# Kernel tuning notes

Measured on AMD Instinct MI355X. Metric: run time of the kernel, lower is better.

The kernel has to match this reference:

```python
import jax, jax.numpy as jnp
import numpy as np

N_NODES = 50000
N_EDGES = 800000
IN_F = 128
HEADS = 8
HEAD_DIM = 16
ALPHA = 0.2  # LeakyReLU negative slope
EPS = 1e-6


def setup_inputs() -> dict:
    key = jax.random.key(0)
    k1, k2, k3, k4 = jax.random.split(key, 4)
    x = jax.random.normal(k1, (N_NODES, IN_F), dtype=jnp.float32)
    edge_index = jax.random.randint(k2, (2, N_EDGES), 0, N_NODES, dtype=jnp.int32)
    std = 1.0 / np.sqrt(IN_F)
    W = jax.random.uniform(k3, (HEADS, IN_F, HEAD_DIM), minval=-std, maxval=std, dtype=jnp.float32)
    a = jax.random.uniform(k4, (HEADS, 2 * HEAD_DIM, 1), minval=-std, maxval=std, dtype=jnp.float32)
    bias = jnp.zeros((HEADS * HEAD_DIM,), dtype=jnp.float32)
    return {"x": x, "edge_index": edge_index, "W": W, "a": a, "bias": bias}


def reference(x, edge_index, W, a, bias):
    N = x.shape[0]
    src = edge_index[0]
    tgt = edge_index[1]
    # per-head linear transform: [N, H, D]
    h = jnp.einsum('nf,hfd->nhd', x, W)
    # split attention vector: a = [a_src; a_tgt], each [H, D]
    a_src = a[:, :HEAD_DIM, 0]
    a_tgt = a[:, HEAD_DIM:, 0]
    # node-level partial scores, then gather (equivalent to concat@a on edges)
    s_node_src = jnp.einsum('nhd,hd->nh', h, a_src)  # [N, H]
    s_node_tgt = jnp.einsum('nhd,hd->nh', h, a_tgt)  # [N, H]
    scores = s_node_src[src] + s_node_tgt[tgt]       # [E, H]
    scores = jnp.where(scores >= 0, scores, ALPHA * scores)  # LeakyReLU
    # edge softmax per target node, per head (global max subtract + clamp, as in source)
    max_per_head = jnp.max(scores, axis=0, keepdims=True)    # [1, H]
    exp_scores = jnp.exp(jnp.clip(scores - max_per_head, -20.0, 20.0))  # [E, H]
    denom = jax.ops.segment_sum(exp_scores, tgt, num_segments=N) + EPS  # [N, H]
    attn = exp_scores / denom[tgt]                                      # [E, H]
    # weighted scatter-add aggregation
    weighted = h[src] * attn[:, :, None]                                # [E, H, D]
    agg = jax.ops.segment_sum(weighted, tgt, num_segments=N)            # [N, H, D]
    out = agg.reshape(N, HEADS * HEAD_DIM) + bias
    return out
```

## Files before the change

### kernel.cpp

```cpp
#include <hip/hip_runtime.h>
#include <stdint.h>

#define N_NODES 50000
#define N_EDGES 800000
#define IN_F 128
#define HEADS 8
#define HEAD_DIM 16
#define ALPHA 0.2f
#define EPSV 1e-6f

#define NB 196
#define CAP 4800

typedef short short8 __attribute__((ext_vector_type(8)));
typedef float floatx4 __attribute__((ext_vector_type(4)));

__device__ __forceinline__ float bflo(unsigned v) {
    return __uint_as_float(v << 16);
}
__device__ __forceinline__ float bfhi(unsigned v) {
    return __uint_as_float(v & 0xffff0000u);
}
__device__ __forceinline__ unsigned f2bf(float f) {
    unsigned u = __float_as_uint(f);
    return (u + 0x7fffu + ((u >> 16) & 1u)) >> 16;
}

__global__ __launch_bounds__(256) void k_wt(const float* __restrict__ W,
                                            ushort* __restrict__ WTb,
                                            int* __restrict__ gcnt) {
    int i = blockIdx.x * 256 + threadIdx.x;
    int c = i >> 7, f = i & 127;
    WTb[i] = (ushort)f2bf(W[(c >> 4) * 2048 + f * 16 + (c & 15)]);
    if (i < NB) gcnt[i] = 0;
}

__global__ __launch_bounds__(256) void k_mid(const float* __restrict__ x,
                                             const ushort* __restrict__ WTb,
                                             const float* __restrict__ a,
                                             ushort* __restrict__ hb,
                                             float* __restrict__ s_src,
                                             float* __restrict__ s_tgt,
                                             const int* __restrict__ srcA,
                                             const int* __restrict__ tgtA,
                                             int* __restrict__ gcnt,
                                             unsigned* __restrict__ bucketbuf) {
    int bi = blockIdx.x;
    int q3 = bi / 3, r3 = bi - q3 * 3;
    int t = threadIdx.x;

    if (r3 == 2) {
        __shared__ int lcnt[NB];
        __shared__ int lbase[NB];
        if (t < NB) lcnt[t] = 0;
        __syncthreads();

        int base = q3 * 2048 + t;
        int tg[8], sr[8];
        bool vld[8];
#pragma unroll
        for (int k = 0; k < 8; k++) {
            int e = base + k * 256;
            vld[k] = (e < N_EDGES);
            int ee = vld[k] ? e : 0;
            tg[k] = tgtA[ee];
            sr[k] = srcA[ee];
        }
#pragma unroll
        for (int k = 0; k < 8; k++)
            if (vld[k]) atomicAdd(&lcnt[tg[k] >> 8], 1);
        __syncthreads();
        if (t < NB) {
            int c = lcnt[t];
            lbase[t] = (c > 0) ? atomicAdd(&gcnt[t], c) : 0;
            lcnt[t] = 0;
        }
        __syncthreads();
#pragma unroll
        for (int k = 0; k < 8; k++) {
            if (vld[k]) {
                int b = tg[k] >> 8;
                int off = atomicAdd(&lcnt[b], 1);
                int pos = lbase[b] + off;
                if (pos < CAP)
                    bucketbuf[(size_t)b * CAP + pos] =
                        ((unsigned)(tg[k] & 255) << 16) | (unsigned)sr[k];
            }
        }
        return;
    }

    int mb = q3 * 2 + r3;
    int wave = t >> 6, lane = t & 63;
    int quad = lane >> 4, col = lane & 15;
    int nb = mb * 64 + wave * 16;

    int na = nb + col;
    int nac = na < N_NODES ? na : (N_NODES - 1);
    const float* xrow = x + (size_t)nac * 128 + quad * 8;

    floatx4 acc[8];
    floatx4 z = {0.f, 0.f, 0.f, 0.f};
#pragma unroll
    for (int ct = 0; ct < 8; ct++) acc[ct] = z;

#pragma unroll
    for (int kc = 0; kc < 4; kc++) {
        float4 f0 = *(const float4*)(xrow + kc * 32);
        float4 f1 = *(const float4*)(xrow + kc * 32 + 4);
        short8 af;
        af[0] = (short)f2bf(f0.x); af[1] = (short)f2bf(f0.y);
        af[2] = (short)f2bf(f0.z); af[3] = (short)f2bf(f0.w);
        af[4] = (short)f2bf(f1.x); af[5] = (short)f2bf(f1.y);
        af[6] = (short)f2bf(f1.z); af[7] = (short)f2bf(f1.w);
#pragma unroll
        for (int ct = 0; ct < 8; ct++) {
            const ushort* wrow = WTb + (size_t)(ct * 16 + col) * 128 + kc * 32 + quad * 8;
            short8 bf = *(const short8*)wrow;
            acc[ct] = __builtin_amdgcn_mfma_f32_16x16x32_bf16(af, bf, acc[ct], 0, 0, 0);
        }
    }

    float af_s[8], af_t[8];
#pragma unroll
    for (int ct = 0; ct < 8; ct++) {
        af_s[ct] = a[ct * 32 + col];
        af_t[ct] = a[ct * 32 + 16 + col];
    }

#pragma unroll
    for (int r = 0; r < 4; r++) {
        int node = nb + quad * 4 + r;
        bool nv = (node < N_NODES);
        if (nv) {
            ushort* hrow = hb + (size_t)node * 128 + col;
#pragma unroll
            for (int ct = 0; ct < 8; ct++)
                hrow[ct * 16] = (ushort)f2bf(acc[ct][r]);
        }
        float ps[8], pt[8];
#pragma unroll
        for (int ct = 0; ct < 8; ct++) {
            float hs = acc[ct][r];
            float vs = hs * af_s[ct];
            float vt = hs * af_t[ct];
#pragma unroll
            for (int off = 1; off < 16; off <<= 1) {
                vs += __shfl_xor(vs, off, 64);
                vt += __shfl_xor(vt, off, 64);
            }
            ps[ct] = vs; pt[ct] = vt;
        }
        if (nv && col == 0) {
            *(float4*)(s_src + (size_t)node * 8)     = make_float4(ps[0], ps[1], ps[2], ps[3]);
            *(float4*)(s_src + (size_t)node * 8 + 4) = make_float4(ps[4], ps[5], ps[6], ps[7]);
            *(float4*)(s_tgt + (size_t)node * 8)     = make_float4(pt[0], pt[1], pt[2], pt[3]);
            *(float4*)(s_tgt + (size_t)node * 8 + 4) = make_float4(pt[4], pt[5], pt[6], pt[7]);
        }
    }
}

__global__ __launch_bounds__(256) void k_passB(const unsigned* __restrict__ bucketbuf,
                                               const int* __restrict__ gcnt,
                                               int* __restrict__ rowptr,
                                               ushort* __restrict__ src16) {
    __shared__ int bin[256];
    __shared__ int wsum[4];
    __shared__ int woff[4];
    __shared__ int sbase;
    __shared__ ushort stage[CAP];
    int t = threadIdx.x, lane = t & 63, w = t >> 6;
    int b = blockIdx.x;

    bin[t] = 0;
    int g = (t < NB) ? gcnt[t] : 0;
    int incg = g;
#pragma unroll
    for (int off = 1; off < 64; off <<= 1) {
        int nn = __shfl_up(incg, off, 64);
        if (lane >= off) incg += nn;
    }
    if (lane == 63) wsum[w] = incg;
    __syncthreads();
    if (t == 0) {
        woff[0] = 0;
        woff[1] = wsum[0];
        woff[2] = wsum[0] + wsum[1];
        woff[3] = wsum[0] + wsum[1] + wsum[2];
    }
    __syncthreads();
    if (t == b) sbase = woff[w] + incg - g;
    if (b == 0 && t == 0) rowptr[N_NODES] = N_EDGES;
    __syncthreads();
    int base = sbase;
    int n = gcnt[b]; if (n > CAP) n = CAP;
    const unsigned* buf = bucketbuf + (size_t)b * CAP;

    for (int i = t; i < n; i += 256)
        atomicAdd(&bin[buf[i] >> 16], 1);
    __syncthreads();
    int v = bin[t];
    int inc = v;
#pragma unroll
    for (int off = 1; off < 64; off <<= 1) {
        int nn = __shfl_up(inc, off, 64);
        if (lane >= off) inc += nn;
    }
    if (lane == 63) wsum[w] = inc;
    __syncthreads();
    if (t == 0) {
        woff[0] = 0;
        woff[1] = wsum[0];
        woff[2] = wsum[0] + wsum[1];
        woff[3] = wsum[0] + wsum[1] + wsum[2];
    }
    __syncthreads();
    int excl = woff[w] + inc - v;
    int node = b * 256 + t;
    if (node < N_NODES) rowptr[node] = base + excl;
    __syncthreads();
    bin[t] = excl;
    __syncthreads();
    for (int i = t; i < n; i += 256) {
        unsigned p = buf[i];
        int off = atomicAdd(&bin[p >> 16], 1);
        stage[off] = (ushort)(p & 0xffffu);
    }
    __syncthreads();
    for (int i = t; i < n; i += 256)
        src16[base + i] = stage[i];
}

__global__ __launch_bounds__(256) void k_fused(const int* __restrict__ rowptr,
                                               const ushort* __restrict__ src16,
                                               const float* __restrict__ s_src,
                                               const float* __restrict__ s_tgt,
                                               const unsigned* __restrict__ h16,
                                               const float* __restrict__ bias,
                                               float* __restrict__ outb) {
    int t = threadIdx.x;
    int wave = t >> 6, lane = t & 63;
    int half = lane >> 5, hl = lane & 31;
    int n = blockIdx.x * 8 + wave * 2 + half;
    int head = hl >> 2;
    int c = 4 * hl;

    const uint2* h2 = (const uint2*)h16;

    float st = s_tgt[n * 8 + head];
    int begin = rowptr[n], end = rowptr[n + 1];

    float ax = 0.f, ay = 0.f, az = 0.f, aw = 0.f, den = 0.f;
    int e = begin;
    for (; e + 7 < end; e += 8) {
        int s0 = src16[e];
        int s1 = src16[e + 1];
        int s2 = src16[e + 2];
        int s3 = src16[e + 3];
        int s4 = src16[e + 4];
        int s5 = src16[e + 5];
        int s6 = src16[e + 6];
        int s7 = src16[e + 7];
        float t0 = s_src[s0 * 8 + head];
        float t1 = s_src[s1 * 8 + head];
        float t2 = s_src[s2 * 8 + head];
        float t3 = s_src[s3 * 8 + head];
        float t4 = s_src[s4 * 8 + head];
        float t5 = s_src[s5 * 8 + head];
        float t6 = s_src[s6 * 8 + head];
        float t7 = s_src[s7 * 8 + head];
        uint2 p0 = h2[s0 * 32 + hl];
        uint2 p1 = h2[s1 * 32 + hl];
        uint2 p2 = h2[s2 * 32 + hl];
        uint2 p3 = h2[s3 * 32 + hl];
        uint2 p4 = h2[s4 * 32 + hl];
        uint2 p5 = h2[s5 * 32 + hl];
        uint2 p6 = h2[s6 * 32 + hl];
        uint2 p7 = h2[s7 * 32 + hl];
        float v0 = t0 + st; v0 = v0 >= 0.f ? v0 : ALPHA * v0;
        float v1 = t1 + st; v1 = v1 >= 0.f ? v1 : ALPHA * v1;
        float v2 = t2 + st; v2 = v2 >= 0.f ? v2 : ALPHA * v2;
        float v3 = t3 + st; v3 = v3 >= 0.f ? v3 : ALPHA * v3;
        float v4 = t4 + st; v4 = v4 >= 0.f ? v4 : ALPHA * v4;
        float v5 = t5 + st; v5 = v5 >= 0.f ? v5 : ALPHA * v5;
        float v6 = t6 + st; v6 = v6 >= 0.f ? v6 : ALPHA * v6;
        float v7 = t7 + st; v7 = v7 >= 0.f ? v7 : ALPHA * v7;
        float x0 = __expf(fminf(fmaxf(v0, -20.f), 20.f));
        float x1 = __expf(fminf(fmaxf(v1, -20.f), 20.f));
        float x2 = __expf(fminf(fmaxf(v2, -20.f), 20.f));
        float x3 = __expf(fminf(fmaxf(v3, -20.f), 20.f));
        float x4 = __expf(fminf(fmaxf(v4, -20.f), 20.f));
        float x5 = __expf(fminf(fmaxf(v5, -20.f), 20.f));
        float x6 = __expf(fminf(fmaxf(v6, -20.f), 20.f));
        float x7 = __expf(fminf(fmaxf(v7, -20.f), 20.f));
        den += ((x0 + x1) + (x2 + x3)) + ((x4 + x5) + (x6 + x7));
        ax = fmaf(x0, bflo(p0.x), fmaf(x1, bflo(p1.x), fmaf(x2, bflo(p2.x), fmaf(x3, bflo(p3.x), ax))));
        ax = fmaf(x4, bflo(p4.x), fmaf(x5, bflo(p5.x), fmaf(x6, bflo(p6.x), fmaf(x7, bflo(p7.x), ax))));
        ay = fmaf(x0, bfhi(p0.x), fmaf(x1, bfhi(p1.x), fmaf(x2, bfhi(p2.x), fmaf(x3, bfhi(p3.x), ay))));
        ay = fmaf(x4, bfhi(p4.x), fmaf(x5, bfhi(p5.x), fmaf(x6, bfhi(p6.x), fmaf(x7, bfhi(p7.x), ay))));
        az = fmaf(x0, bflo(p0.y), fmaf(x1, bflo(p1.y), fmaf(x2, bflo(p2.y), fmaf(x3, bflo(p3.y), az))));
        az = fmaf(x4, bflo(p4.y), fmaf(x5, bflo(p5.y), fmaf(x6, bflo(p6.y), fmaf(x7, bflo(p7.y), az))));
        aw = fmaf(x0, bfhi(p0.y), fmaf(x1, bfhi(p1.y), fmaf(x2, bfhi(p2.y), fmaf(x3, bfhi(p3.y), aw))));
        aw = fmaf(x4, bfhi(p4.y), fmaf(x5, bfhi(p5.y), fmaf(x6, bfhi(p6.y), fmaf(x7, bfhi(p7.y), aw))));
    }
    if (e + 3 < end) {
        int s0 = src16[e];
        int s1 = src16[e + 1];
        int s2 = src16[e + 2];
        int s3 = src16[e + 3];
        float t0 = s_src[s0 * 8 + head];
        float t1 = s_src[s1 * 8 + head];
        float t2 = s_src[s2 * 8 + head];
        float t3 = s_src[s3 * 8 + head];
        uint2 p0 = h2[s0 * 32 + hl];
        uint2 p1 = h2[s1 * 32 + hl];
        uint2 p2 = h2[s2 * 32 + hl];
        uint2 p3 = h2[s3 * 32 + hl];
        float v0 = t0 + st; v0 = v0 >= 0.f ? v0 : ALPHA * v0;
        float v1 = t1 + st; v1 = v1 >= 0.f ? v1 : ALPHA * v1;
        float v2 = t2 + st; v2 = v2 >= 0.f ? v2 : ALPHA * v2;
        float v3 = t3 + st; v3 = v3 >= 0.f ? v3 : ALPHA * v3;
        float x0 = __expf(fminf(fmaxf(v0, -20.f), 20.f));
        float x1 = __expf(fminf(fmaxf(v1, -20.f), 20.f));
        float x2 = __expf(fminf(fmaxf(v2, -20.f), 20.f));
        float x3 = __expf(fminf(fmaxf(v3, -20.f), 20.f));
        den += (x0 + x1) + (x2 + x3);
        ax = fmaf(x0, bflo(p0.x), fmaf(x1, bflo(p1.x), fmaf(x2, bflo(p2.x), fmaf(x3, bflo(p3.x), ax))));
        ay = fmaf(x0, bfhi(p0.x), fmaf(x1, bfhi(p1.x), fmaf(x2, bfhi(p2.x), fmaf(x3, bfhi(p3.x), ay))));
        az = fmaf(x0, bflo(p0.y), fmaf(x1, bflo(p1.y), fmaf(x2, bflo(p2.y), fmaf(x3, bflo(p3.y), az))));
        aw = fmaf(x0, bfhi(p0.y), fmaf(x1, bfhi(p1.y), fmaf(x2, bfhi(p2.y), fmaf(x3, bfhi(p3.y), aw))));
        e += 4;
    }
    for (; e < end; e++) {
        int sA = src16[e];
        float ssA = s_src[sA * 8 + head];
        uint2 pA = h2[sA * 32 + hl];
        float vA = ssA + st; vA = vA >= 0.f ? vA : ALPHA * vA;
        float exA = __expf(fminf(fmaxf(vA, -20.f), 20.f));
        den += exA;
        ax = fmaf(exA, bflo(pA.x), ax);
        ay = fmaf(exA, bfhi(pA.x), ay);
        az = fmaf(exA, bflo(pA.y), az);
        aw = fmaf(exA, bfhi(pA.y), aw);
    }
    float r = 1.f / (den + EPSV);
    float4 b = *(const float4*)(bias + c);
    float4 o;
    o.x = fmaf(ax, r, b.x);
    o.y = fmaf(ay, r, b.y);
    o.z = fmaf(az, r, b.z);
    o.w = fmaf(aw, r, b.w);
    *(float4*)(outb + (size_t)n * 128 + c) = o;
}

extern "C" void kernel_launch(void* const* d_in, const int* in_sizes, int n_in,
                              void* d_out, int out_size, void* d_ws, size_t ws_size,
                              hipStream_t stream) {
    const float* x    = (const float*)d_in[0];
    const int*   ei   = (const int*)d_in[1];
    const float* W    = (const float*)d_in[2];
    const float* a    = (const float*)d_in[3];
    const float* bias = (const float*)d_in[4];
    float* outb = (float*)d_out;

    char* ws = (char*)d_ws;
    ushort* hb        = (ushort*)(ws);
    float* s_src      = (float*)(ws + 12800000);
    float* s_tgt      = (float*)(ws + 14400000);
    int*   rowptr     = (int*)  (ws + 16000000);
    ushort* src16     = (ushort*)(ws + 16200064);
    int*   gcnt       = (int*)  (ws + 17800064);
    ushort* WTb       = (ushort*)(ws + 17902528);
    unsigned* bucketbuf = (unsigned*)(ws + 17935296);

    const int* srcA = ei;
    const int* tgtA = ei + N_EDGES;

    hipLaunchKernelGGL(k_wt,    dim3(64),   dim3(256), 0, stream, W, WTb, gcnt);
    hipLaunchKernelGGL(k_mid,   dim3(1173), dim3(256), 0, stream,
                       x, WTb, a, hb, s_src, s_tgt, srcA, tgtA, gcnt, bucketbuf);
    hipLaunchKernelGGL(k_passB, dim3(196),  dim3(256), 0, stream, bucketbuf, gcnt, rowptr, src16);
    hipLaunchKernelGGL(k_fused, dim3(6250), dim3(256), 0, stream, rowptr, src16, s_src, s_tgt, (const unsigned*)hb, bias, outb);
}
```

Measured before the change: 156.6 us.

## Regroup stages: bucket edges first, then overlap GEMM with CSR build

The W transpose moves into an extra block of a new edge-bucketing kernel, and the GEMM is co-scheduled with the per-bucket CSR build (passB) inside one kernel using a 4:1 block interleave. The edge bucketing now runs before the GEMM and uses 1024 edges per block instead of 2048. The goal is to cut one launch, hide the CSR build behind the MFMA work, and fill more blocks in the bucketing pass. In exchange it adds a memset launch, and the bucketing pass is no longer hidden behind the GEMM.

```diff
diff --git a/kernel.cpp b/kernel.cpp
--- a/kernel.cpp
+++ b/kernel.cpp
@@ -26,74 +26,146 @@
     return (u + 0x7fffu + ((u >> 16) & 1u)) >> 16;
 }
 
-__global__ __launch_bounds__(256) void k_wt(const float* __restrict__ W,
-                                            ushort* __restrict__ WTb,
-                                            int* __restrict__ gcnt) {
-    int i = blockIdx.x * 256 + threadIdx.x;
-    int c = i >> 7, f = i & 127;
-    WTb[i] = (ushort)f2bf(W[(c >> 4) * 2048 + f * 16 + (c & 15)]);
-    if (i < NB) gcnt[i] = 0;
-}
-
-__global__ __launch_bounds__(256) void k_mid(const float* __restrict__ x,
-                                             const ushort* __restrict__ WTb,
-                                             const float* __restrict__ a,
-                                             ushort* __restrict__ hb,
-                                             float* __restrict__ s_src,
-                                             float* __restrict__ s_tgt,
-                                             const int* __restrict__ srcA,
-                                             const int* __restrict__ tgtA,
-                                             int* __restrict__ gcnt,
-                                             unsigned* __restrict__ bucketbuf) {
+__global__ __launch_bounds__(256) void k_front(const int* __restrict__ srcA,
+                                               const int* __restrict__ tgtA,
+                                               int* __restrict__ gcnt,
+                                               unsigned* __restrict__ bucketbuf,
+                                               const float* __restrict__ W,
+                                               ushort* __restrict__ WTb) {
+    int b = blockIdx.x, t = threadIdx.x;
+    if (b == 782) {
+        for (int i = t; i < 16384; i += 256) {
+            int c = i >> 7, f = i & 127;
+            WTb[i] = (ushort)f2bf(W[(c >> 4) * 2048 + f * 16 + (c & 15)]);
+        }
+        return;
+    }
+    __shared__ int lcnt[NB];
+    __shared__ int lbase[NB];
+    if (t < NB) lcnt[t] = 0;
+    __syncthreads();
+
+    int base = b * 1024 + t;
+    int tg[4], sr[4];
+    bool vld[4];
+#pragma unroll
+    for (int k = 0; k < 4; k++) {
+        int e = base + k * 256;
+        vld[k] = (e < N_EDGES);
+        int ee = vld[k] ? e : 0;
+        tg[k] = tgtA[ee];
+        sr[k] = srcA[ee];
+    }
+#pragma unroll
+    for (int k = 0; k < 4; k++)
+        if (vld[k]) atomicAdd(&lcnt[tg[k] >> 8], 1);
+    __syncthreads();
+    if (t < NB) {
+        int c = lcnt[t];
+        lbase[t] = (c > 0) ? atomicAdd(&gcnt[t], c) : 0;
+        lcnt[t] = 0;
+    }
+    __syncthreads();
+#pragma unroll
+    for (int k = 0; k < 4; k++) {
+        if (vld[k]) {
+            int bb = tg[k] >> 8;
+            int off = atomicAdd(&lcnt[bb], 1);
+            int pos = lbase[bb] + off;
+            if (pos < CAP)
+                bucketbuf[(size_t)bb * CAP + pos] =
+                    ((unsigned)(tg[k] & 255) << 16) | (unsigned)sr[k];
+        }
+    }
+}
+
+__global__ __launch_bounds__(256) void k_mid2(const float* __restrict__ x,
+                                              const ushort* __restrict__ WTb,
+                                              const float* __restrict__ a,
+                                              ushort* __restrict__ hb,
+                                              float* __restrict__ s_src,
+                                              float* __restrict__ s_tgt,
+                                              const unsigned* __restrict__ bucketbuf,
+                                              const int* __restrict__ gcnt,
+                                              int* __restrict__ rowptr,
+                                              ushort* __restrict__ src16) {
     int bi = blockIdx.x;
-    int q3 = bi / 3, r3 = bi - q3 * 3;
-    int t = threadIdx.x;
-
-    if (r3 == 2) {
-        __shared__ int lcnt[NB];
-        __shared__ int lbase[NB];
-        if (t < NB) lcnt[t] = 0;
-        __syncthreads();
-
-        int base = q3 * 2048 + t;
-        int tg[8], sr[8];
-        bool vld[8];
-#pragma unroll
-        for (int k = 0; k < 8; k++) {
-            int e = base + k * 256;
-            vld[k] = (e < N_EDGES);
-            int ee = vld[k] ? e : 0;
-            tg[k] = tgtA[ee];
-            sr[k] = srcA[ee];
-        }
-#pragma unroll
-        for (int k = 0; k < 8; k++)
-            if (vld[k]) atomicAdd(&lcnt[tg[k] >> 8], 1);
-        __syncthreads();
-        if (t < NB) {
-            int c = lcnt[t];
-            lbase[t] = (c > 0) ? atomicAdd(&gcnt[t], c) : 0;
-            lcnt[t] = 0;
-        }
-        __syncthreads();
-#pragma unroll
-        for (int k = 0; k < 8; k++) {
-            if (vld[k]) {
-                int b = tg[k] >> 8;
-                int off = atomicAdd(&lcnt[b], 1);
-                int pos = lbase[b] + off;
-                if (pos < CAP)
-                    bucketbuf[(size_t)b * CAP + pos] =
-                        ((unsigned)(tg[k] & 255) << 16) | (unsigned)sr[k];
-            }
-        }
+    int q = bi / 5, r = bi - q * 5;
+    int t = threadIdx.x, lane = t & 63, w = t >> 6;
+
+    if (r == 4) {
+        __shared__ int bin[256];
+        __shared__ int wsum[4];
+        __shared__ int woff[4];
+        __shared__ int sbase;
+        __shared__ ushort stage[CAP];
+        int b = q;
+
+        bin[t] = 0;
+        int g = (t < NB) ? gcnt[t] : 0;
+        int incg = g;
+#pragma unroll
+        for (int off = 1; off < 64; off <<= 1) {
+            int nn = __shfl_up(incg, off, 64);
+            if (lane >= off) incg += nn;
+        }
+        if (lane == 63) wsum[w] = incg;
+        __syncthreads();
+        if (t == 0) {
+            woff[0] = 0;
+            woff[1] = wsum[0];
+            woff[2] = wsum[0] + wsum[1];
+            woff[3] = wsum[0] + wsum[1] + wsum[2];
+        }
+        __syncthreads();
+        if (t == b) sbase = woff[w] + incg - g;
+        if (b == 0 && t == 0) rowptr[N_NODES] = N_EDGES;
+        __syncthreads();
+        int base = sbase;
+        int n = gcnt[b]; if (n > CAP) n = CAP;
+        const unsigned* buf = bucketbuf + (size_t)b * CAP;
+
+        for (int i = t; i < n; i += 256)
+            atomicAdd(&bin[buf[i] >> 16], 1);
+        __syncthreads();
+        int v = bin[t];
+        int inc = v;
+#pragma unroll
+        for (int off = 1; off < 64; off <<= 1) {
+            int nn = __shfl_up(inc, off, 64);
+            if (lane >= off) inc += nn;
+        }
+        if (lane == 63) wsum[w] = inc;
+        __syncthreads();
+        if (t == 0) {
+            woff[0] = 0;
+            woff[1] = wsum[0];
+            woff[2] = wsum[0] + wsum[1];
+            woff[3] = wsum[0] + wsum[1] + wsum[2];
+        }
+        __syncthreads();
+        int excl = woff[w] + inc - v;
+        int node = b * 256 + t;
+        if (node < N_NODES) rowptr[node] = base + excl;
+        __syncthreads();
+        bin[t] = excl;
+        __syncthreads();
+        for (int i = t; i < n; i += 256) {
+            unsigned p = buf[i];
+            int off = atomicAdd(&bin[p >> 16], 1);
+            stage[off] = (ushort)(p & 0xffffu);
+        }
+        __syncthreads();
+        for (int i = t; i < n; i += 256)
+            src16[base + i] = stage[i];
         return;
     }
 
-    int mb = q3 * 2 + r3;
-    int wave = t >> 6, lane = t & 63;
+    int mb = q * 4 + r;
+    int wave = w;
     int quad = lane >> 4, col = lane & 15;
     int nb = mb * 64 + wave * 16;
+    if (mb * 64 >= N_NODES) return;
 
     int na = nb + col;
     int nac = na < N_NODES ? na : (N_NODES - 1);
@@ -129,19 +201,19 @@
     }
 
 #pragma unroll
-    for (int r = 0; r < 4; r++) {
-        int node = nb + quad * 4 + r;
+    for (int rr = 0; rr < 4; rr++) {
+        int node = nb + quad * 4 + rr;
         bool nv = (node < N_NODES);
         if (nv) {
             ushort* hrow = hb + (size_t)node * 128 + col;
 #pragma unroll
             for (int ct = 0; ct < 8; ct++)
-                hrow[ct * 16] = (ushort)f2bf(acc[ct][r]);
+                hrow[ct * 16] = (ushort)f2bf(acc[ct][rr]);
         }
         float ps[8], pt[8];
 #pragma unroll
         for (int ct = 0; ct < 8; ct++) {
-            float hs = acc[ct][r];
+            float hs = acc[ct][rr];
             float vs = hs * af_s[ct];
             float vt = hs * af_t[ct];
 #pragma unroll
@@ -158,77 +230,6 @@
             *(float4*)(s_tgt + (size_t)node * 8 + 4) = make_float4(pt[4], pt[5], pt[6], pt[7]);
         }
     }
-}
-
-__global__ __launch_bounds__(256) void k_passB(const unsigned* __restrict__ bucketbuf,
-                                               const int* __restrict__ gcnt,
-                                               int* __restrict__ rowptr,
-                                               ushort* __restrict__ src16) {
-    __shared__ int bin[256];
-    __shared__ int wsum[4];
-    __shared__ int woff[4];
-    __shared__ int sbase;
-    __shared__ ushort stage[CAP];
-    int t = threadIdx.x, lane = t & 63, w = t >> 6;
-    int b = blockIdx.x;
-
-    bin[t] = 0;
-    int g = (t < NB) ? gcnt[t] : 0;
-    int incg = g;
-#pragma unroll
-    for (int off = 1; off < 64; off <<= 1) {
-        int nn = __shfl_up(incg, off, 64);
-        if (lane >= off) incg += nn;
-    }
-    if (lane == 63) wsum[w] = incg;
-    __syncthreads();
-    if (t == 0) {
-        woff[0] = 0;
-        woff[1] = wsum[0];
-        woff[2] = wsum[0] + wsum[1];
-        woff[3] = wsum[0] + wsum[1] + wsum[2];
-    }
-    __syncthreads();
-    if (t == b) sbase = woff[w] + incg - g;
-    if (b == 0 && t == 0) rowptr[N_NODES] = N_EDGES;
-    __syncthreads();
-    int base = sbase;
-    int n = gcnt[b]; if (n > CAP) n = CAP;
-    const unsigned* buf = bucketbuf + (size_t)b * CAP;
-
-    for (int i = t; i < n; i += 256)
-        atomicAdd(&bin[buf[i] >> 16], 1);
-    __syncthreads();
-    int v = bin[t];
-    int inc = v;
-#pragma unroll
-    for (int off = 1; off < 64; off <<= 1) {
-        int nn = __shfl_up(inc, off, 64);
-        if (lane >= off) inc += nn;
-    }
-    if (lane == 63) wsum[w] = inc;
-    __syncthreads();
-    if (t == 0) {
-        woff[0] = 0;
-        woff[1] = wsum[0];
-        woff[2] = wsum[0] + wsum[1];
-        woff[3] = wsum[0] + wsum[1] + wsum[2];
-    }
-    __syncthreads();
-    int excl = woff[w] + inc - v;
-    int node = b * 256 + t;
-    if (node < N_NODES) rowptr[node] = base + excl;
-    __syncthreads();
-    bin[t] = excl;
-    __syncthreads();
-    for (int i = t; i < n; i += 256) {
-        unsigned p = buf[i];
-        int off = atomicAdd(&bin[p >> 16], 1);
-        stage[off] = (ushort)(p & 0xffffu);
-    }
-    __syncthreads();
-    for (int i = t; i < n; i += 256)
-        src16[base + i] = stage[i];
 }
 
 __global__ __launch_bounds__(256) void k_fused(const int* __restrict__ rowptr,
@@ -376,9 +377,9 @@
     const int* srcA = ei;
     const int* tgtA = ei + N_EDGES;
 
-    hipLaunchKernelGGL(k_wt,    dim3(64),   dim3(256), 0, stream, W, WTb, gcnt);
-    hipLaunchKernelGGL(k_mid,   dim3(1173), dim3(256), 0, stream,
-                       x, WTb, a, hb, s_src, s_tgt, srcA, tgtA, gcnt, bucketbuf);
-    hipLaunchKernelGGL(k_passB, dim3(196),  dim3(256), 0, stream, bucketbuf, gcnt, rowptr, src16);
+    hipMemsetAsync(gcnt, 0, NB * sizeof(int), stream);
+    hipLaunchKernelGGL(k_front, dim3(783),  dim3(256), 0, stream, srcA, tgtA, gcnt, bucketbuf, W, WTb);
+    hipLaunchKernelGGL(k_mid2,  dim3(980),  dim3(256), 0, stream,
+                       x, WTb, a, hb, s_src, s_tgt, bucketbuf, gcnt, rowptr, src16);
     hipLaunchKernelGGL(k_fused, dim3(6250), dim3(256), 0, stream, rowptr, src16, s_src, s_tgt, (const unsigned*)hb, bias, outb);
 }
```

Measured after the change: 169.9 us. 8.5% more time.
